# Kernel optimization log

Hardware: AMD Instinct MI355X
Metric: run time of the kernel (lower is better)

## Reference

```python
import jax, jax.numpy as jnp
import numpy as np

POOL = 7              # roi_size (output bins per side)
SAMPLING_RATIO = 2    # bilinear samples per bin side
POOLED_DIM = 5        # CEM_FILTER(245) // (7*7)
SPATIAL_SCALE = 0.0625  # 1/16 feature stride


def setup_inputs() -> dict:
    key = jax.random.key(0)
    k1, k2, k3 = jax.random.split(key, 3)
    B, C, H, W = 8, 245, 100, 100
    N = 512
    IMG = 1600.0
    x = jax.random.normal(k1, (B, C, H, W), dtype=jnp.float32)
    xy = jax.random.uniform(k2, (B, N, 2), minval=0.0, maxval=IMG - 256.0)
    wh = jax.random.uniform(k3, (B, N, 2), minval=16.0, maxval=256.0)
    boxes = jnp.concatenate([xy, xy + wh], axis=-1)  # (x1,y1,x2,y2) in image coords
    return {"x": x, "boxes": boxes}


def reference(x, boxes):
    """Position-sensitive RoIAlign (torchvision ps_roi_align semantics).
    x: [B, C=POOLED_DIM*POOL*POOL, H, W]; boxes: [B, N, 4] in image coords.
    Returns [B*N, POOLED_DIM, POOL, POOL]."""
    B, C, H, W = x.shape
    Bb, N, _ = boxes.shape
    R = Bb * N
    g, P, D, s = SAMPLING_RATIO, POOL, POOLED_DIM, SPATIAL_SCALE

    batch_idx = jnp.repeat(jnp.arange(Bb, dtype=jnp.int32), N)  # convert_to_roi_format ids
    rois = boxes.reshape(R, 4)

    # aligned roi coords on the feature map (half-pixel offset)
    start_w = rois[:, 0] * s - 0.5
    start_h = rois[:, 1] * s - 0.5
    end_w = rois[:, 2] * s - 0.5
    end_h = rois[:, 3] * s - 0.5
    bin_h = (end_h - start_h) / P
    bin_w = (end_w - start_w) / P

    p = jnp.arange(P, dtype=jnp.float32)
    i = jnp.arange(g, dtype=jnp.float32)
    # sample coordinates, shape [R, P, g]
    ys = start_h[:, None, None] + p[None, :, None] * bin_h[:, None, None] \
         + (i[None, None, :] + 0.5) * bin_h[:, None, None] / g
    xs = start_w[:, None, None] + p[None, :, None] * bin_w[:, None, None] \
         + (i[None, None, :] + 0.5) * bin_w[:, None, None] / g

    # zero outside [-1, H] / [-1, W] (torchvision bilinear_interpolate)
    vy = ((ys >= -1.0) & (ys <= H)).astype(x.dtype)  # [R,P,g]
    vx = ((xs >= -1.0) & (xs <= W)).astype(x.dtype)

    yc = jnp.clip(ys, 0.0, H - 1.0)
    xc = jnp.clip(xs, 0.0, W - 1.0)
    yl = jnp.floor(yc).astype(jnp.int32)
    xl = jnp.floor(xc).astype(jnp.int32)
    yh = jnp.minimum(yl + 1, H - 1)
    xh = jnp.minimum(xl + 1, W - 1)
    ly = yc - yl.astype(x.dtype); hy = 1.0 - ly
    lx = xc - xl.astype(x.dtype); hx = 1.0 - lx

    # position-sensitive input channel: c_in = (d*P + ph)*P + pw, shape [D,P,P]
    c_in = ((jnp.arange(D)[:, None, None] * P + jnp.arange(P)[None, :, None]) * P
            + jnp.arange(P)[None, None, :]).astype(jnp.int32)

    # broadcast to [R, D, P(h), P(w), g(h), g(w)]
    b = batch_idx[:, None, None, None, None, None]
    c = c_in[None, :, :, :, None, None]
    gy = lambda a: a[:, None, :, None, :, None]  # y-axis arrays [R,P,g]
    gx = lambda a: a[:, None, None, :, None, :]  # x-axis arrays [R,P,g]

    v11 = x[b, c, gy(yl), gx(xl)]
    v12 = x[b, c, gy(yl), gx(xh)]
    v21 = x[b, c, gy(yh), gx(xl)]
    v22 = x[b, c, gy(yh), gx(xh)]
    val = (gy(hy) * gx(hx) * v11 + gy(hy) * gx(lx) * v12
           + gy(ly) * gx(hx) * v21 + gy(ly) * gx(lx) * v22)
    val = val * (gy(vy) * gx(vx))
    out = val.sum(axis=(4, 5)) / (g * g)  # average over sampling grid -> [R, D, P, P]
    return out
```

## Files before the change

### kernel.cpp

```cpp
#include <hip/hip_runtime.h>

#define POOL 7
#define SCALE 0.0625f
#define HW 10000
#define NROI 512
#define NCH 245
#define JJ 64

typedef const __attribute__((address_space(1))) void* gas_ptr;
typedef __attribute__((address_space(3))) void* las_ptr;

__global__ __launch_bounds__(512) void psroi_kernel(
    const float* __restrict__ x, const float* __restrict__ boxes,
    float* __restrict__ out)
{
    __shared__ float plane[2][HW + 4];

    const int H = 100, W = 100;
    int bid = blockIdx.x;
    int b = bid & 7;
    int j = bid >> 3;
    int npl = (j < 53) ? 4 : 3;

    int n = threadIdx.x;
    int r = b * NROI + n;
    int lane = threadIdx.x & 63;
    int wave = threadIdx.x >> 6;

    const float* xb = x + (size_t)b * NCH * HW;

    auto stage = [&](int buf, int c) {
        const float4* src4 = (const float4*)(xb + (size_t)c * HW);
        #pragma unroll
        for (int i = 0; i < 5; ++i) {
            int chunk_base = i * 512 + wave * 64;
            int chunk = chunk_base + lane;
            if (chunk < HW / 4) {
                __builtin_amdgcn_global_load_lds(
                    (gas_ptr)(src4 + chunk),
                    (las_ptr)((char*)&plane[buf][0] + (size_t)chunk_base * 16),
                    16, 0, 0);
            }
        }
    };

    float4 bx = *(const float4*)(boxes + (size_t)r * 4);
    stage(0, j);
    if (threadIdx.x < 8)
        plane[threadIdx.x >> 2][HW + (threadIdx.x & 3)] = 0.f;

    float sw = bx.x * SCALE - 0.5f;
    float sh = bx.y * SCALE - 0.5f;
    float bin_h = (bx.w * SCALE - 0.5f - sh) / (float)POOL;
    float bin_w = (bx.z * SCALE - 0.5f - sw) / (float)POOL;

    __syncthreads();

    for (int t = 0; t < npl; ++t) {
        int c = j + JJ * t;
        bool pre = (t + 1 < npl);
        if (pre) stage((t + 1) & 1, j + JJ * (t + 1));

        int ph = (c / POOL) % POOL;
        int pw = c % POOL;
        float fy0 = sh + (float)ph * bin_h;
        float fx0 = sw + (float)pw * bin_w;

        int   rowa[2], rstep[2];
        float wyh[2], wyl[2];
        #pragma unroll
        for (int iy = 0; iy < 2; ++iy) {
            float y  = fy0 + ((float)iy + 0.5f) * bin_h * 0.5f;
            float vy = (y >= -1.0f && y <= (float)H) ? 1.0f : 0.0f;
            float yc = fminf(fmaxf(y, 0.0f), (float)(H - 1));
            int   yl = (int)floorf(yc);
            float ly = yc - (float)yl;
            wyl[iy] = ly * vy;
            wyh[iy] = (1.0f - ly) * vy;
            rowa[iy]  = yl * W;
            rstep[iy] = (yl < H - 1) ? W : 0;
        }
        int   colx[2];
        float wxh[2], wxl[2];
        #pragma unroll
        for (int ix = 0; ix < 2; ++ix) {
            float xf = fx0 + ((float)ix + 0.5f) * bin_w * 0.5f;
            float vx = (xf >= -1.0f && xf <= (float)W) ? 1.0f : 0.0f;
            float xc = fminf(fmaxf(xf, 0.0f), (float)(W - 1));
            int   xl = (int)floorf(xc);
            float lx = xc - (float)xl;
            wxl[ix] = lx * vx;
            wxh[ix] = (1.0f - lx) * vx;
            colx[ix] = xl;
        }

        if (pre) asm volatile("s_waitcnt vmcnt(5)" ::: "memory");
        else     asm volatile("s_waitcnt vmcnt(0)" ::: "memory");
        __builtin_amdgcn_s_barrier();

        const float* pl = &plane[t & 1][0];
        float sum = 0.f;
        #pragma unroll
        for (int iy = 0; iy < 2; ++iy) {
            #pragma unroll
            for (int ix = 0; ix < 2; ++ix) {
                int a0 = rowa[iy] + colx[ix];
                int a1 = a0 + rstep[iy];
                float v11 = pl[a0];
                float v12 = pl[a0 + 1];
                float v21 = pl[a1];
                float v22 = pl[a1 + 1];
                float top = wxh[ix] * v11 + wxl[ix] * v12;
                float bot = wxh[ix] * v21 + wxl[ix] * v22;
                sum = fmaf(wyh[iy], top, sum);
                sum = fmaf(wyl[iy], bot, sum);
            }
        }
        out[(size_t)r * NCH + c] = sum * 0.25f;

        __builtin_amdgcn_s_barrier();
    }
}

extern "C" void kernel_launch(void* const* d_in, const int* in_sizes, int n_in,
                              void* d_out, int out_size, void* d_ws, size_t ws_size,
                              hipStream_t stream) {
    const float* x     = (const float*)d_in[0];
    const float* boxes = (const float*)d_in[1];
    float* out = (float*)d_out;

    (void)in_sizes; (void)n_in; (void)out_size; (void)d_ws; (void)ws_size;

    hipLaunchKernelGGL(psroi_kernel, dim3(8 * JJ), dim3(512), 0, stream,
                       x, boxes, out);
}
```

Baseline: 19.83 us.

## Triple-buffer channel planes with two-ahead prefetch and fewer, longer blocks

Cuts the grid from 512 to 256 blocks, so each block now processes 7-8 channel planes instead of 3-4. Shared memory grows to three plane buffers so loads are issued two planes ahead, with vmcnt waits adjusted to match. Results are held in registers and written out after the loop, so the output stores no longer sit inside the barrier-synchronised loop. The extra LDS use (about 120KB) may allow only one block per CU, and with 256 blocks some CUs may sit idle.

```diff
diff --git a/kernel.cpp b/kernel.cpp
--- a/kernel.cpp
+++ b/kernel.cpp
@@ -5,7 +5,8 @@
 #define HW 10000
 #define NROI 512
 #define NCH 245
-#define JJ 64
+#define SSTRIDE 32
+#define MAXPL 8
 
 typedef const __attribute__((address_space(1))) void* gas_ptr;
 typedef __attribute__((address_space(3))) void* las_ptr;
@@ -14,19 +15,18 @@
     const float* __restrict__ x, const float* __restrict__ boxes,
     float* __restrict__ out)
 {
-    __shared__ float plane[2][HW + 4];
+    __shared__ float plane[3][HW + 4];
+    const int H = 100, W = 100;
 
-    const int H = 100, W = 100;
     int bid = blockIdx.x;
     int b = bid & 7;
-    int j = bid >> 3;
-    int npl = (j < 53) ? 4 : 3;
+    int s = bid >> 3;
+    int np = (s < 21) ? 8 : 7;
 
     int n = threadIdx.x;
     int r = b * NROI + n;
     int lane = threadIdx.x & 63;
     int wave = threadIdx.x >> 6;
-
     const float* xb = x + (size_t)b * NCH * HW;
 
     auto stage = [&](int buf, int c) {
@@ -45,8 +45,9 @@
     };
 
     float4 bx = *(const float4*)(boxes + (size_t)r * 4);
-    stage(0, j);
-    if (threadIdx.x < 8)
+    stage(0, s);
+    stage(1, s + SSTRIDE);
+    if (threadIdx.x < 12)
         plane[threadIdx.x >> 2][HW + (threadIdx.x & 3)] = 0.f;
 
     float sw = bx.x * SCALE - 0.5f;
@@ -54,13 +55,14 @@
     float bin_h = (bx.w * SCALE - 0.5f - sh) / (float)POOL;
     float bin_w = (bx.z * SCALE - 0.5f - sw) / (float)POOL;
 
-    __syncthreads();
+    float res[MAXPL];
 
-    for (int t = 0; t < npl; ++t) {
-        int c = j + JJ * t;
-        bool pre = (t + 1 < npl);
-        if (pre) stage((t + 1) & 1, j + JJ * (t + 1));
+    #pragma unroll
+    for (int t = 0; t < MAXPL; ++t) {
+        if (t >= np) break;
+        if (t + 2 < np) stage((t + 2) % 3, s + SSTRIDE * (t + 2));
 
+        int c = s + SSTRIDE * t;
         int ph = (c / POOL) % POOL;
         int pw = c % POOL;
         float fy0 = sh + (float)ph * bin_h;
@@ -94,11 +96,17 @@
             colx[ix] = xl;
         }
 
-        if (pre) asm volatile("s_waitcnt vmcnt(5)" ::: "memory");
-        else     asm volatile("s_waitcnt vmcnt(0)" ::: "memory");
+        int ahead = np - 1 - t; if (ahead > 2) ahead = 2;
+        if (ahead == 2)
+            asm volatile("s_waitcnt vmcnt(10) lgkmcnt(0)" ::: "memory");
+        else if (ahead == 1)
+            asm volatile("s_waitcnt vmcnt(5) lgkmcnt(0)" ::: "memory");
+        else
+            asm volatile("s_waitcnt vmcnt(0) lgkmcnt(0)" ::: "memory");
+        __builtin_amdgcn_sched_barrier(0);
         __builtin_amdgcn_s_barrier();
 
-        const float* pl = &plane[t & 1][0];
+        const float* pl = &plane[t % 3][0];
         float sum = 0.f;
         #pragma unroll
         for (int iy = 0; iy < 2; ++iy) {
@@ -116,9 +124,16 @@
                 sum = fmaf(wyl[iy], bot, sum);
             }
         }
-        out[(size_t)r * NCH + c] = sum * 0.25f;
+        res[t] = sum * 0.25f;
 
         __builtin_amdgcn_s_barrier();
+    }
+
+    float* outr = out + (size_t)r * NCH + s;
+    #pragma unroll
+    for (int t = 0; t < MAXPL; ++t) {
+        if (t >= np) break;
+        outr[SSTRIDE * t] = res[t];
     }
 }
 
@@ -131,6 +146,6 @@
 
     (void)in_sizes; (void)n_in; (void)out_size; (void)d_ws; (void)ws_size;
 
-    hipLaunchKernelGGL(psroi_kernel, dim3(8 * JJ), dim3(512), 0, stream,
+    hipLaunchKernelGGL(psroi_kernel, dim3(256), dim3(512), 0, stream,
                        x, boxes, out);
 }
```

Result: slower. 23.70 us (+19.5%).

## Replace per-block double-buffered channel loop with two channels per 1024-thread block

Applied to the files above, without the earlier changes.

Each block now handles two channels at once with 1024 threads: each half of the block stages its own channel plane into LDS and all 512 ROIs are sampled in a single pass. The multi-iteration software pipeline with its barriers and vmcnt waits is removed, and the grid grows from 512 to 984 blocks. This is meant to expose more parallelism and cut per-block serialization. In exchange it loses the overlap between loading the next plane and computing the current one, and about 80KB of LDS per block limits residency.

```diff
diff --git a/kernel.cpp b/kernel.cpp
--- a/kernel.cpp
+++ b/kernel.cpp
@@ -3,34 +3,40 @@
 #define POOL 7
 #define SCALE 0.0625f
 #define HW 10000
+#define PLSZ 10004
 #define NROI 512
 #define NCH 245
-#define JJ 64
 
 typedef const __attribute__((address_space(1))) void* gas_ptr;
 typedef __attribute__((address_space(3))) void* las_ptr;
 
-__global__ __launch_bounds__(512) void psroi_kernel(
+__global__ __launch_bounds__(1024) void psroi_kernel(
     const float* __restrict__ x, const float* __restrict__ boxes,
     float* __restrict__ out)
 {
-    __shared__ float plane[2][HW + 4];
+    __shared__ float plane[2][PLSZ];
+    const int H = 100, W = 100;
 
-    const int H = 100, W = 100;
     int bid = blockIdx.x;
     int b = bid & 7;
-    int j = bid >> 3;
-    int npl = (j < 53) ? 4 : 3;
+    int k = bid >> 3;
+    int c0 = 2 * k;
 
-    int n = threadIdx.x;
+    int g = threadIdx.x >> 9;
+    int n = threadIdx.x & 511;
+    int c = c0 + g;
+    bool act = (c < NCH);
+
     int r = b * NROI + n;
     int lane = threadIdx.x & 63;
-    int wave = threadIdx.x >> 6;
-
+    int wave = (threadIdx.x >> 6) & 7;
     const float* xb = x + (size_t)b * NCH * HW;
 
-    auto stage = [&](int buf, int c) {
+    float4 bx = *(const float4*)(boxes + (size_t)r * 4);
+
+    if (act) {
         const float4* src4 = (const float4*)(xb + (size_t)c * HW);
+        char* lds = (char*)&plane[g][0];
         #pragma unroll
         for (int i = 0; i < 5; ++i) {
             int chunk_base = i * 512 + wave * 64;
@@ -38,14 +44,11 @@
             if (chunk < HW / 4) {
                 __builtin_amdgcn_global_load_lds(
                     (gas_ptr)(src4 + chunk),
-                    (las_ptr)((char*)&plane[buf][0] + (size_t)chunk_base * 16),
+                    (las_ptr)(lds + (size_t)chunk_base * 16),
                     16, 0, 0);
             }
         }
-    };
-
-    float4 bx = *(const float4*)(boxes + (size_t)r * 4);
-    stage(0, j);
+    }
     if (threadIdx.x < 8)
         plane[threadIdx.x >> 2][HW + (threadIdx.x & 3)] = 0.f;
 
@@ -54,72 +57,62 @@
     float bin_h = (bx.w * SCALE - 0.5f - sh) / (float)POOL;
     float bin_w = (bx.z * SCALE - 0.5f - sw) / (float)POOL;
 
+    int ph = (c / POOL) % POOL;
+    int pw = c % POOL;
+    float fy0 = sh + (float)ph * bin_h;
+    float fx0 = sw + (float)pw * bin_w;
+
+    int   rowa[2], rstep[2];
+    float wyh[2], wyl[2];
+    #pragma unroll
+    for (int iy = 0; iy < 2; ++iy) {
+        float y  = fy0 + ((float)iy + 0.5f) * bin_h * 0.5f;
+        float vy = (y >= -1.0f && y <= (float)H) ? 1.0f : 0.0f;
+        float yc = fminf(fmaxf(y, 0.0f), (float)(H - 1));
+        int   yl = (int)floorf(yc);
+        float ly = yc - (float)yl;
+        wyl[iy] = ly * vy;
+        wyh[iy] = (1.0f - ly) * vy;
+        rowa[iy]  = yl * W;
+        rstep[iy] = (yl < H - 1) ? W : 0;
+    }
+    int   colx[2];
+    float wxh[2], wxl[2];
+    #pragma unroll
+    for (int ix = 0; ix < 2; ++ix) {
+        float xf = fx0 + ((float)ix + 0.5f) * bin_w * 0.5f;
+        float vx = (xf >= -1.0f && xf <= (float)W) ? 1.0f : 0.0f;
+        float xc = fminf(fmaxf(xf, 0.0f), (float)(W - 1));
+        int   xl = (int)floorf(xc);
+        float lx = xc - (float)xl;
+        wxl[ix] = lx * vx;
+        wxh[ix] = (1.0f - lx) * vx;
+        colx[ix] = xl;
+    }
+
     __syncthreads();
 
-    for (int t = 0; t < npl; ++t) {
-        int c = j + JJ * t;
-        bool pre = (t + 1 < npl);
-        if (pre) stage((t + 1) & 1, j + JJ * (t + 1));
+    if (!act) return;
 
-        int ph = (c / POOL) % POOL;
-        int pw = c % POOL;
-        float fy0 = sh + (float)ph * bin_h;
-        float fx0 = sw + (float)pw * bin_w;
-
-        int   rowa[2], rstep[2];
-        float wyh[2], wyl[2];
-        #pragma unroll
-        for (int iy = 0; iy < 2; ++iy) {
-            float y  = fy0 + ((float)iy + 0.5f) * bin_h * 0.5f;
-            float vy = (y >= -1.0f && y <= (float)H) ? 1.0f : 0.0f;
-            float yc = fminf(fmaxf(y, 0.0f), (float)(H - 1));
-            int   yl = (int)floorf(yc);
-            float ly = yc - (float)yl;
-            wyl[iy] = ly * vy;
-            wyh[iy] = (1.0f - ly) * vy;
-            rowa[iy]  = yl * W;
-            rstep[iy] = (yl < H - 1) ? W : 0;
-        }
-        int   colx[2];
-        float wxh[2], wxl[2];
+    const float* pl = &plane[g][0];
+    float sum = 0.f;
+    #pragma unroll
+    for (int iy = 0; iy < 2; ++iy) {
         #pragma unroll
         for (int ix = 0; ix < 2; ++ix) {
-            float xf = fx0 + ((float)ix + 0.5f) * bin_w * 0.5f;
-            float vx = (xf >= -1.0f && xf <= (float)W) ? 1.0f : 0.0f;
-            float xc = fminf(fmaxf(xf, 0.0f), (float)(W - 1));
-            int   xl = (int)floorf(xc);
-            float lx = xc - (float)xl;
-            wxl[ix] = lx * vx;
-            wxh[ix] = (1.0f - lx) * vx;
-            colx[ix] = xl;
+            int a0 = rowa[iy] + colx[ix];
+            int a1 = a0 + rstep[iy];
+            float v11 = pl[a0];
+            float v12 = pl[a0 + 1];
+            float v21 = pl[a1];
+            float v22 = pl[a1 + 1];
+            float top = wxh[ix] * v11 + wxl[ix] * v12;
+            float bot = wxh[ix] * v21 + wxl[ix] * v22;
+            sum = fmaf(wyh[iy], top, sum);
+            sum = fmaf(wyl[iy], bot, sum);
         }
-
-        if (pre) asm volatile("s_waitcnt vmcnt(5)" ::: "memory");
-        else     asm volatile("s_waitcnt vmcnt(0)" ::: "memory");
-        __builtin_amdgcn_s_barrier();
-
-        const float* pl = &plane[t & 1][0];
-        float sum = 0.f;
-        #pragma unroll
-        for (int iy = 0; iy < 2; ++iy) {
-            #pragma unroll
-            for (int ix = 0; ix < 2; ++ix) {
-                int a0 = rowa[iy] + colx[ix];
-                int a1 = a0 + rstep[iy];
-                float v11 = pl[a0];
-                float v12 = pl[a0 + 1];
-                float v21 = pl[a1];
-                float v22 = pl[a1 + 1];
-                float top = wxh[ix] * v11 + wxl[ix] * v12;
-                float bot = wxh[ix] * v21 + wxl[ix] * v22;
-                sum = fmaf(wyh[iy], top, sum);
-                sum = fmaf(wyl[iy], bot, sum);
-            }
-        }
-        out[(size_t)r * NCH + c] = sum * 0.25f;
-
-        __builtin_amdgcn_s_barrier();
     }
+    out[(size_t)r * NCH + c] = sum * 0.25f;
 }
 
 extern "C" void kernel_launch(void* const* d_in, const int* in_sizes, int n_in,
@@ -131,6 +124,6 @@
 
     (void)in_sizes; (void)n_in; (void)out_size; (void)d_ws; (void)ws_size;
 
-    hipLaunchKernelGGL(psroi_kernel, dim3(8 * JJ), dim3(512), 0, stream,
+    hipLaunchKernelGGL(psroi_kernel, dim3(8 * 123), dim3(1024), 0, stream,
                        x, boxes, out);
 }
```

Measured after the change: 20.21 us. No clear change (+1.9%).
